# Kernel tuning notes

Measured on AMD Instinct MI355X. Metric: run time of the kernel, lower is better.

## Reference

```python
import jax, jax.numpy as jnp
import numpy as np

P, F_IN, HG, C, T, E, HOUT = 4096, 64, 64, 64, 32, 65536, 12
LEAKY_SLOPE = 0.2
LN_EPS = 1e-5


def setup_inputs() -> dict:
    key = jax.random.key(0)
    ks = jax.random.split(key, 14)
    g = lambda k, shape, scale: (jax.random.normal(k, shape, jnp.float32) * scale)
    return {
        "X": jax.random.normal(ks[0], (1, P, F_IN, T), jnp.float32),
        "edge_index": jax.random.randint(ks[1], (T, 2, E), 0, P, jnp.int32),
        # GATv2 params (single head)
        "Wl": g(ks[2], (F_IN, HG), 0.1),
        "Wr": g(ks[3], (F_IN, HG), 0.1),
        "att": g(ks[4], (HG,), 0.1),
        "gat_b": g(ks[5], (HG,), 0.02),
        # 1x1 time conv (HG -> C) and 1x1 residual conv (F_IN -> C)
        "W_time": g(ks[6], (C, HG), 0.1),
        "b_time": g(ks[7], (C,), 0.02),
        "W_res": g(ks[8], (C, F_IN), 0.1),
        "b_res": g(ks[9], (C,), 0.02),
        # LayerNorm over channel dim C
        "ln_g": jnp.ones((C,), jnp.float32),
        "ln_b": jnp.zeros((C,), jnp.float32),
        # final conv: Conv2d(in=T, out=HOUT, kernel=(1, C)) -> weight (HOUT, T, C)
        "W_final": g(ks[10], (HOUT, T, C), 0.05),
        "b_final": g(ks[11], (HOUT,), 0.02),
    }


def reference(X, edge_index, Wl, Wr, att, gat_b, W_time, b_time, W_res, b_res,
              ln_g, ln_b, W_final, b_final):
    Pn = X.shape[1]

    def gat_t(x, edges):
        # x: (P, F_IN), edges: (2, E) with edges[0]=src j, edges[1]=dst i
        src, dst = edges[0], edges[1]
        hl = x @ Wl                      # (P, HG) messages
        hr = x @ Wr                      # (P, HG) query side
        e = jax.nn.leaky_relu(hl[src] + hr[dst], LEAKY_SLOPE) @ att  # (E,)
        emax = jax.ops.segment_max(e, dst, num_segments=Pn)
        ex = jnp.exp(e - emax[dst])
        den = jax.ops.segment_sum(ex, dst, num_segments=Pn)
        alpha = ex / den[dst]            # softmax over in-edges of each dst
        return jax.ops.segment_sum(alpha[:, None] * hl[src], dst,
                                   num_segments=Pn) + gat_b  # (P, HG)

    xs = jnp.moveaxis(X[0], -1, 0)                     # (T, P, F_IN)
    X_hat = jax.nn.relu(jax.vmap(gat_t)(xs, edge_index))  # (T, P, HG)

    th = jnp.einsum('tph,ch->tpc', X_hat, W_time) + b_time  # time conv 1x1
    rs = jnp.einsum('tpf,cf->tpc', xs, W_res) + b_res       # residual conv 1x1
    y = jax.nn.relu(th + rs)                                 # (T, P, C)

    mu = jnp.mean(y, axis=-1, keepdims=True)
    var = jnp.var(y, axis=-1, keepdims=True)
    yn = (y - mu) * jax.lax.rsqrt(var + LN_EPS) * ln_g + ln_b  # (T, P, C)

    # final conv: in-channels = T, kernel (1, C) -> contract over t and c
    out = jnp.einsum('tpc,otc->po', yn, W_final) + b_final     # (P, HOUT)
    return out[None]                                           # (1, P, HOUT)
```

## Files before the change

### kernel.cpp

```cpp
#include <hip/hip_runtime.h>
#include <math.h>

#define NP 4096
#define F_IN 64
#define HG 64
#define NC 64
#define NT 32
#define NE 65536
#define HOUT 12
#define LEAKY 0.2f
#define LN_EPS 1e-5f
#define CAP 48

template <int CTRL>
__device__ __forceinline__ float dppadd(float v, float x) {
    int r = __builtin_amdgcn_update_dpp(0, __builtin_bit_cast(int, x), CTRL, 0xF, 0xF, false);
    return v + __builtin_bit_cast(float, r);
}
__device__ __forceinline__ float rowsum16(float v) {
    v = dppadd<0x128>(v, v);
    v = dppadd<0x124>(v, v);
    v = dppadd<0x122>(v, v);
    v = dppadd<0x121>(v, v);
    return v;
}
__device__ __forceinline__ float laneXorSum(float v) {
    v += __shfl_xor(v, 16, 64);
    v += __shfl_xor(v, 32, 64);
    return v;
}

#define FMA4(Acomp, B, r)                                                     \
    acc[r][0] += (Acomp) * (B).x; acc[r][1] += (Acomp) * (B).y;               \
    acc[r][2] += (Acomp) * (B).z; acc[r][3] += (Acomp) * (B).w;

__global__ __launch_bounds__(256) void k_front(const float* __restrict__ X,
        const float* __restrict__ Wl, const float* __restrict__ Wr,
        const float* __restrict__ W_res, const float* __restrict__ b_res,
        const float* __restrict__ W_time, const float* __restrict__ bf,
        float* __restrict__ hl, float* __restrict__ hr, float* __restrict__ rs,
        float* __restrict__ wtT, float* __restrict__ out) {
    __shared__ float smem[8960];
    int b = blockIdx.x;
    int tid = threadIdx.x;
    if (b < 2048) {
        float (*xs)[F_IN][36] = (float (*)[F_IN][36])smem;
        float (*bk)[68] = (float (*)[68])(smem + 4608);
        int p0 = b * 2;
        const float4* Xp = (const float4*)(X + (size_t)p0 * F_IN * NT);
        for (int i4 = tid; i4 < 1024; i4 += 256) {
            int pp = i4 >> 9, f = (i4 >> 3) & 63, t0 = (i4 & 7) * 4;
            *(float4*)&xs[pp][f][t0] = Xp[i4];
        }
        int ng = tid & 15, pp = (tid >> 4) & 1, tg = tid >> 5;
        int n0 = ng * 4, t0 = tg * 4;
        {
            const float4* B4 = (const float4*)Wl;
            for (int i4 = tid; i4 < 1024; i4 += 256)
                *(float4*)&bk[i4 >> 4][(i4 & 15) * 4] = B4[i4];
            __syncthreads();
            float acc[4][4];
#pragma unroll
            for (int i = 0; i < 4; ++i)
#pragma unroll
                for (int j2 = 0; j2 < 4; ++j2) acc[i][j2] = 0.f;
#pragma unroll 8
            for (int f = 0; f < F_IN; ++f) {
                float4 B = *(const float4*)&bk[f][n0];
                float4 A = *(const float4*)&xs[pp][f][t0];
                FMA4(A.x, B, 0) FMA4(A.y, B, 1) FMA4(A.z, B, 2) FMA4(A.w, B, 3)
            }
#pragma unroll
            for (int i = 0; i < 4; ++i) {
                float4 v;
                v.x = acc[i][0]; v.y = acc[i][1]; v.z = acc[i][2]; v.w = acc[i][3];
                *(float4*)&hl[((size_t)(t0 + i) * NP + p0 + pp) * HG + n0] = v;
            }
            __syncthreads();
        }
        {
            const float4* B4 = (const float4*)Wr;
            for (int i4 = tid; i4 < 1024; i4 += 256)
                *(float4*)&bk[i4 >> 4][(i4 & 15) * 4] = B4[i4];
            __syncthreads();
            float acc[4][4];
#pragma unroll
            for (int i = 0; i < 4; ++i)
#pragma unroll
                for (int j2 = 0; j2 < 4; ++j2) acc[i][j2] = 0.f;
#pragma unroll 8
            for (int f = 0; f < F_IN; ++f) {
                float4 B = *(const float4*)&bk[f][n0];
                float4 A = *(const float4*)&xs[pp][f][t0];
                FMA4(A.x, B, 0) FMA4(A.y, B, 1) FMA4(A.z, B, 2) FMA4(A.w, B, 3)
            }
#pragma unroll
            for (int i = 0; i < 4; ++i) {
                float4 v;
                v.x = acc[i][0]; v.y = acc[i][1]; v.z = acc[i][2]; v.w = acc[i][3];
                *(float4*)&hr[((size_t)(t0 + i) * NP + p0 + pp) * HG + n0] = v;
            }
            __syncthreads();
        }
        {
            for (int i = tid; i < F_IN * NC; i += 256) {
                int c = i >> 6, f = i & 63;
                bk[f][c] = W_res[i];
            }
            __syncthreads();
            float4 br4 = *(const float4*)&b_res[n0];
            float acc[4][4];
#pragma unroll
            for (int i = 0; i < 4; ++i) {
                acc[i][0] = br4.x; acc[i][1] = br4.y; acc[i][2] = br4.z; acc[i][3] = br4.w;
            }
#pragma unroll 8
            for (int f = 0; f < F_IN; ++f) {
                float4 B = *(const float4*)&bk[f][n0];
                float4 A = *(const float4*)&xs[pp][f][t0];
                FMA4(A.x, B, 0) FMA4(A.y, B, 1) FMA4(A.z, B, 2) FMA4(A.w, B, 3)
            }
#pragma unroll
            for (int i = 0; i < 4; ++i) {
                float4 v;
                v.x = acc[i][0]; v.y = acc[i][1]; v.z = acc[i][2]; v.w = acc[i][3];
                *(float4*)&rs[((size_t)(t0 + i) * NP + p0 + pp) * NC + n0] = v;
            }
        }
    } else if (b < 2064) {
        int i = (b - 2048) * 256 + tid;
        wtT[i] = W_time[(i & 63) * 64 + (i >> 6)];
    } else {
        int i = (b - 2064) * 256 + tid;
        out[i] = bf[i % HOUT];
    }
}

__global__ __launch_bounds__(512) void k_build(const int* __restrict__ EI,
        int* __restrict__ cnt, unsigned short* __restrict__ scap) {
    __shared__ unsigned short buck[512][CAP];
    __shared__ int cnts[512];
    int b = blockIdx.x;
    int t = (b & 7) + 8 * ((b >> 3) & 3);
    int r = b >> 5;
    int tid = threadIdx.x;
    cnts[tid] = 0;
    __syncthreads();
    const int4* srcA = (const int4*)(EI + (size_t)t * 2 * NE);
    const int4* dstA = (const int4*)(EI + (size_t)t * 2 * NE + NE);
    for (int i = tid; i < NE / 4; i += 512) {
        int4 s = srcA[i];
        int4 d = dstA[i];
        if ((d.x >> 9) == r) { int lo = d.x & 511; int sl = atomicAdd(&cnts[lo], 1); if (sl < CAP) buck[lo][sl] = (unsigned short)s.x; }
        if ((d.y >> 9) == r) { int lo = d.y & 511; int sl = atomicAdd(&cnts[lo], 1); if (sl < CAP) buck[lo][sl] = (unsigned short)s.y; }
        if ((d.z >> 9) == r) { int lo = d.z & 511; int sl = atomicAdd(&cnts[lo], 1); if (sl < CAP) buck[lo][sl] = (unsigned short)s.z; }
        if ((d.w >> 9) == r) { int lo = d.w & 511; int sl = atomicAdd(&cnts[lo], 1); if (sl < CAP) buck[lo][sl] = (unsigned short)s.w; }
    }
    __syncthreads();
    cnt[(t << 12) + (r << 9) + tid] = cnts[tid];
    unsigned int* dstw = (unsigned int*)(scap + ((size_t)((t << 12) + (r << 9))) * CAP);
    const unsigned int* srcw = (const unsigned int*)buck;
    for (int i = tid; i < 512 * CAP / 2; i += 512)
        dstw[i] = srcw[i];
}

__global__ __launch_bounds__(256) void k_gat(const float* __restrict__ hl,
        float* __restrict__ hr,
        const int* __restrict__ cnt, const unsigned short* __restrict__ scap,
        const float* __restrict__ att, const float* __restrict__ gat_b) {
    __shared__ int sidx[4][64];
    int b = blockIdx.x;
    int k = b >> 3;
    int t = (b & 7) + 8 * (k >> 10);
    int ws = threadIdx.x >> 6;
    int i = (k & 1023) * 4 + ws;
    int lane = threadIdx.x & 63;
    int row = lane >> 4;
    int c0 = (lane & 15) * 4;
    size_t nbase = ((size_t)t * NP + i) * HG;
    const float* hlt = hl + (size_t)t * NP * HG;
    float4 r4 = *(const float4*)&hr[nbase + c0];
    float4 at4 = *(const float4*)&att[c0];
    int deg = cnt[(t << 12) + i];
    deg = (deg < CAP) ? deg : CAP;
    const unsigned short* sp = scap + ((size_t)((t << 12) + i)) * CAP;
    int stage = (lane < deg) ? lane : 0;
    sidx[ws][lane] = (int)sp[stage];
    float l = 0.f;
    float4 acc = {0.f, 0.f, 0.f, 0.f};
    int nfull = deg & ~7;
    int j = 0;
    for (; j < nfull; j += 8) {
        int src0 = sidx[ws][j + row];
        int src1 = sidx[ws][j + 4 + row];
        float4 h0 = *(const float4*)&hlt[((size_t)src0 << 6) + c0];
        float4 h1 = *(const float4*)&hlt[((size_t)src1 << 6) + c0];
        float4 z0, z1;
        z0.x = h0.x + r4.x; z0.y = h0.y + r4.y; z0.z = h0.z + r4.z; z0.w = h0.w + r4.w;
        z1.x = h1.x + r4.x; z1.y = h1.y + r4.y; z1.z = h1.z + r4.z; z1.w = h1.w + r4.w;
        z0.x = fmaxf(z0.x, LEAKY * z0.x); z0.y = fmaxf(z0.y, LEAKY * z0.y);
        z0.z = fmaxf(z0.z, LEAKY * z0.z); z0.w = fmaxf(z0.w, LEAKY * z0.w);
        z1.x = fmaxf(z1.x, LEAKY * z1.x); z1.y = fmaxf(z1.y, LEAKY * z1.y);
        z1.z = fmaxf(z1.z, LEAKY * z1.z); z1.w = fmaxf(z1.w, LEAKY * z1.w);
        float e0 = rowsum16(z0.x * at4.x + z0.y * at4.y + z0.z * at4.z + z0.w * at4.w);
        float e1 = rowsum16(z1.x * at4.x + z1.y * at4.y + z1.z * at4.z + z1.w * at4.w);
        float w0 = __expf(e0);
        float w1 = __expf(e1);
        l += w0 + w1;
        acc.x += w0 * h0.x + w1 * h1.x;
        acc.y += w0 * h0.y + w1 * h1.y;
        acc.z += w0 * h0.z + w1 * h1.z;
        acc.w += w0 * h0.w + w1 * h1.w;
    }
    for (; j < deg; j += 4) {
        int jj = j + row;
        int src = sidx[ws][(jj < deg) ? jj : 0];
        float4 ha = *(const float4*)&hlt[((size_t)src << 6) + c0];
        float4 za;
        za.x = ha.x + r4.x; za.y = ha.y + r4.y; za.z = ha.z + r4.z; za.w = ha.w + r4.w;
        za.x = fmaxf(za.x, LEAKY * za.x);
        za.y = fmaxf(za.y, LEAKY * za.y);
        za.z = fmaxf(za.z, LEAKY * za.z);
        za.w = fmaxf(za.w, LEAKY * za.w);
        float ep = za.x * at4.x + za.y * at4.y + za.z * at4.z + za.w * at4.w;
        float e = rowsum16(ep);
        float w = __expf(e);
        w = (jj < deg) ? w : 0.f;
        l += w;
        acc.x += w * ha.x; acc.y += w * ha.y; acc.z += w * ha.z; acc.w += w * ha.w;
    }
    float lt = laneXorSum(l);
    acc.x = laneXorSum(acc.x);
    acc.y = laneXorSum(acc.y);
    acc.z = laneXorSum(acc.z);
    acc.w = laneXorSum(acc.w);
    if (row == 0) {
        float inv = (deg > 0) ? (1.0f / lt) : 0.f;
        float4 gb = *(const float4*)&gat_b[c0];
        float4 o;
        o.x = fmaxf(acc.x * inv + gb.x, 0.f);
        o.y = fmaxf(acc.y * inv + gb.y, 0.f);
        o.z = fmaxf(acc.z * inv + gb.z, 0.f);
        o.w = fmaxf(acc.w * inv + gb.w, 0.f);
        *(float4*)&hr[nbase + c0] = o;
    }
}

__global__ __launch_bounds__(256) void k_pf(const float* __restrict__ Xhat,
        const float* __restrict__ wtT, const float* __restrict__ b_time,
        const float* __restrict__ rs, const float* __restrict__ ln_g,
        const float* __restrict__ ln_b, const float* __restrict__ Wf,
        float* __restrict__ out) {
    __shared__ float in_t[64][68];
    __shared__ float bk[64][68];
    int bx = blockIdx.x;
    int tc = bx & 7;
    int p0 = (bx >> 3) * 64;
    int tid = threadIdx.x;
    const float4* wsrc = (const float4*)wtT;
    for (int i4 = tid; i4 < 1024; i4 += 256) {
        int h = i4 >> 4, c4 = (i4 & 15) * 4;
        *(float4*)&bk[h][c4] = wsrc[i4];
    }
    int cg = tid & 15, pg = tid >> 4;
    int c0 = cg * 4, pl = pg * 4;
    float4 bt4 = *(const float4*)&b_time[c0];
    float4 lg = *(const float4*)&ln_g[c0];
    float4 lb = *(const float4*)&ln_b[c0];
    float ot[4][HOUT];
#pragma unroll
    for (int i = 0; i < 4; ++i)
#pragma unroll
        for (int o = 0; o < HOUT; ++o) ot[i][o] = 0.f;
    for (int ti = 0; ti < 4; ++ti) {
        int t = tc + ti * 8;
        __syncthreads();
        const float4* src = (const float4*)(Xhat + ((size_t)t * NP + p0) * HG);
        for (int i4 = tid; i4 < 1024; i4 += 256) {
            int pp = i4 >> 4, c4 = (i4 & 15) * 4;
            *(float4*)&in_t[pp][c4] = src[i4];
        }
        __syncthreads();
        float acc[4][4];
#pragma unroll
        for (int i = 0; i < 4; ++i) {
            acc[i][0] = bt4.x; acc[i][1] = bt4.y; acc[i][2] = bt4.z; acc[i][3] = bt4.w;
        }
#pragma unroll
        for (int k4 = 0; k4 < 16; ++k4) {
            float4 A0 = *(const float4*)&in_t[pl + 0][k4 * 4];
            float4 A1 = *(const float4*)&in_t[pl + 1][k4 * 4];
            float4 A2 = *(const float4*)&in_t[pl + 2][k4 * 4];
            float4 A3 = *(const float4*)&in_t[pl + 3][k4 * 4];
            float4 B0 = *(const float4*)&bk[k4 * 4 + 0][c0];
            FMA4(A0.x, B0, 0) FMA4(A1.x, B0, 1) FMA4(A2.x, B0, 2) FMA4(A3.x, B0, 3)
            float4 B1 = *(const float4*)&bk[k4 * 4 + 1][c0];
            FMA4(A0.y, B1, 0) FMA4(A1.y, B1, 1) FMA4(A2.y, B1, 2) FMA4(A3.y, B1, 3)
            float4 B2 = *(const float4*)&bk[k4 * 4 + 2][c0];
            FMA4(A0.z, B2, 0) FMA4(A1.z, B2, 1) FMA4(A2.z, B2, 2) FMA4(A3.z, B2, 3)
            float4 B3 = *(const float4*)&bk[k4 * 4 + 3][c0];
            FMA4(A0.w, B3, 0) FMA4(A1.w, B3, 1) FMA4(A2.w, B3, 2) FMA4(A3.w, B3, 3)
        }
        float4 ynv[4];
#pragma unroll
        for (int i = 0; i < 4; ++i) {
            size_t prow = (size_t)t * NP + p0 + pl + i;
            float4 r4 = *(const float4*)&rs[prow * NC + c0];
            float y0 = fmaxf(acc[i][0] + r4.x, 0.f), y1 = fmaxf(acc[i][1] + r4.y, 0.f);
            float y2 = fmaxf(acc[i][2] + r4.z, 0.f), y3 = fmaxf(acc[i][3] + r4.w, 0.f);
            float s = rowsum16(y0 + y1 + y2 + y3);
            float ss = rowsum16(y0 * y0 + y1 * y1 + y2 * y2 + y3 * y3);
            float mu = s * (1.f / 64.f);
            float var = ss * (1.f / 64.f) - mu * mu;
            float rsd = rsqrtf(var + LN_EPS);
            ynv[i].x = (y0 - mu) * rsd * lg.x + lb.x;
            ynv[i].y = (y1 - mu) * rsd * lg.y + lb.y;
            ynv[i].z = (y2 - mu) * rsd * lg.z + lb.z;
            ynv[i].w = (y3 - mu) * rsd * lg.w + lb.w;
        }
#pragma unroll
        for (int o = 0; o < HOUT; ++o) {
            float4 w4 = *(const float4*)&Wf[(size_t)o * NT * NC + t * NC + c0];
#pragma unroll
            for (int i = 0; i < 4; ++i)
                ot[i][o] += ynv[i].x * w4.x + ynv[i].y * w4.y
                          + ynv[i].z * w4.z + ynv[i].w * w4.w;
        }
    }
#pragma unroll
    for (int i = 0; i < 4; ++i)
#pragma unroll
        for (int o = 0; o < HOUT; ++o) ot[i][o] = rowsum16(ot[i][o]);
    if (cg == 0) {
#pragma unroll
        for (int i = 0; i < 4; ++i) {
            int p = p0 + pl + i;
#pragma unroll
            for (int o = 0; o < HOUT; ++o)
                atomicAdd(&out[p * HOUT + o], ot[i][o]);
        }
    }
}

extern "C" void kernel_launch(void* const* d_in, const int* in_sizes, int n_in,
                              void* d_out, int out_size, void* d_ws, size_t ws_size,
                              hipStream_t stream) {
    const float* X      = (const float*)d_in[0];
    const int*   EI     = (const int*)d_in[1];
    const float* Wl     = (const float*)d_in[2];
    const float* Wr     = (const float*)d_in[3];
    const float* att    = (const float*)d_in[4];
    const float* gat_b  = (const float*)d_in[5];
    const float* W_time = (const float*)d_in[6];
    const float* b_time = (const float*)d_in[7];
    const float* W_res  = (const float*)d_in[8];
    const float* b_res  = (const float*)d_in[9];
    const float* ln_g   = (const float*)d_in[10];
    const float* ln_b   = (const float*)d_in[11];
    const float* Wf     = (const float*)d_in[12];
    const float* bf     = (const float*)d_in[13];
    float* out = (float*)d_out;

    char* ws = (char*)d_ws;
    const size_t MB = 1024 * 1024;
    float* hl   = (float*)(ws);
    float* hr   = (float*)(ws + 32 * MB);
    float* rs   = (float*)(ws + 64 * MB);
    int*   cnt  = (int*)  (ws + 96 * MB);
    float* wtT  = (float*)(ws + 96 * MB + 512 * 1024);
    unsigned short* scap = (unsigned short*)(ws + 97 * MB);

    k_front<<<2256, 256, 0, stream>>>(X, Wl, Wr, W_res, b_res, W_time, bf,
                                      hl, hr, rs, wtT, out);
    k_build<<<256, 512, 0, stream>>>(EI, cnt, scap);
    k_gat  <<<(NT * NP) / 4, 256, 0, stream>>>(hl, hr, cnt, scap, att, gat_b);
    k_pf   <<<512, 256, 0, stream>>>(hr, wtT, b_time, rs, ln_g, ln_b, Wf, out);
}
```

Baseline: 283.5 us.

## Fuse edge-bucket build into front kernel with split edge halves, widen final pass

Moves the CSR-style in-edge bucket construction into the front kernel as extra 256-thread blocks, so one launch disappears and the edge sorting overlaps with the projection GEMMs. Each block now scans half of the edge list into its own 32-slot bucket, and the GAT kernel merges the two halves per destination, capping total degree at 64. The final projection kernel is also split over 16 time groups instead of 8, doubling its block count. In exchange the GAT kernel does more index arithmetic, and the final kernel issues more atomic adds to the output.

```diff
diff --git a/kernel.cpp b/kernel.cpp
--- a/kernel.cpp
+++ b/kernel.cpp
@@ -10,7 +10,7 @@
 #define HOUT 12
 #define LEAKY 0.2f
 #define LN_EPS 1e-5f
-#define CAP 48
+#define CAPC 32
 
 template <int CTRL>
 __device__ __forceinline__ float dppadd(float v, float x) {
@@ -38,15 +38,43 @@
         const float* __restrict__ Wl, const float* __restrict__ Wr,
         const float* __restrict__ W_res, const float* __restrict__ b_res,
         const float* __restrict__ W_time, const float* __restrict__ bf,
+        const int* __restrict__ EI,
         float* __restrict__ hl, float* __restrict__ hr, float* __restrict__ rs,
-        float* __restrict__ wtT, float* __restrict__ out) {
+        float* __restrict__ wtT, float* __restrict__ out,
+        int* __restrict__ cnt, unsigned short* __restrict__ scap) {
     __shared__ float smem[8960];
     int b = blockIdx.x;
     int tid = threadIdx.x;
-    if (b < 2048) {
+    if (b < 512) {
+        unsigned short (*buck)[CAPC] = (unsigned short (*)[CAPC])smem;
+        int* cnts = (int*)(smem + 8192);
+        int t = (b & 7) + 8 * ((b >> 3) & 3);
+        int rem = b >> 5;
+        int c = rem & 1, r = rem >> 1;
+        cnts[tid] = 0; cnts[tid + 256] = 0;
+        __syncthreads();
+        const int4* srcA = (const int4*)(EI + (size_t)t * 2 * NE) + c * (NE / 8);
+        const int4* dstA = (const int4*)(EI + (size_t)t * 2 * NE + NE) + c * (NE / 8);
+        for (int i = tid; i < NE / 8; i += 256) {
+            int4 s = srcA[i];
+            int4 d = dstA[i];
+            if ((d.x >> 9) == r) { int lo = d.x & 511; int sl = atomicAdd(&cnts[lo], 1); if (sl < CAPC) buck[lo][sl] = (unsigned short)s.x; }
+            if ((d.y >> 9) == r) { int lo = d.y & 511; int sl = atomicAdd(&cnts[lo], 1); if (sl < CAPC) buck[lo][sl] = (unsigned short)s.y; }
+            if ((d.z >> 9) == r) { int lo = d.z & 511; int sl = atomicAdd(&cnts[lo], 1); if (sl < CAPC) buck[lo][sl] = (unsigned short)s.z; }
+            if ((d.w >> 9) == r) { int lo = d.w & 511; int sl = atomicAdd(&cnts[lo], 1); if (sl < CAPC) buck[lo][sl] = (unsigned short)s.w; }
+        }
+        __syncthreads();
+        int obase = ((t * 2 + c) << 12) + (r << 9);
+        cnt[obase + tid] = cnts[tid];
+        cnt[obase + tid + 256] = cnts[tid + 256];
+        unsigned int* dstw = (unsigned int*)(scap + (size_t)obase * CAPC);
+        const unsigned int* srcw = (const unsigned int*)buck;
+        for (int i = tid; i < 512 * CAPC / 2; i += 256)
+            dstw[i] = srcw[i];
+    } else if (b < 2560) {
         float (*xs)[F_IN][36] = (float (*)[F_IN][36])smem;
         float (*bk)[68] = (float (*)[68])(smem + 4608);
-        int p0 = b * 2;
+        int p0 = (b - 512) * 2;
         const float4* Xp = (const float4*)(X + (size_t)p0 * F_IN * NT);
         for (int i4 = tid; i4 < 1024; i4 += 256) {
             int pp = i4 >> 9, f = (i4 >> 3) & 63, t0 = (i4 & 7) * 4;
@@ -127,41 +155,13 @@
                 *(float4*)&rs[((size_t)(t0 + i) * NP + p0 + pp) * NC + n0] = v;
             }
         }
-    } else if (b < 2064) {
-        int i = (b - 2048) * 256 + tid;
+    } else if (b < 2576) {
+        int i = (b - 2560) * 256 + tid;
         wtT[i] = W_time[(i & 63) * 64 + (i >> 6)];
     } else {
-        int i = (b - 2064) * 256 + tid;
+        int i = (b - 2576) * 256 + tid;
         out[i] = bf[i % HOUT];
     }
-}
-
-__global__ __launch_bounds__(512) void k_build(const int* __restrict__ EI,
-        int* __restrict__ cnt, unsigned short* __restrict__ scap) {
-    __shared__ unsigned short buck[512][CAP];
-    __shared__ int cnts[512];
-    int b = blockIdx.x;
-    int t = (b & 7) + 8 * ((b >> 3) & 3);
-    int r = b >> 5;
-    int tid = threadIdx.x;
-    cnts[tid] = 0;
-    __syncthreads();
-    const int4* srcA = (const int4*)(EI + (size_t)t * 2 * NE);
-    const int4* dstA = (const int4*)(EI + (size_t)t * 2 * NE + NE);
-    for (int i = tid; i < NE / 4; i += 512) {
-        int4 s = srcA[i];
-        int4 d = dstA[i];
-        if ((d.x >> 9) == r) { int lo = d.x & 511; int sl = atomicAdd(&cnts[lo], 1); if (sl < CAP) buck[lo][sl] = (unsigned short)s.x; }
-        if ((d.y >> 9) == r) { int lo = d.y & 511; int sl = atomicAdd(&cnts[lo], 1); if (sl < CAP) buck[lo][sl] = (unsigned short)s.y; }
-        if ((d.z >> 9) == r) { int lo = d.z & 511; int sl = atomicAdd(&cnts[lo], 1); if (sl < CAP) buck[lo][sl] = (unsigned short)s.z; }
-        if ((d.w >> 9) == r) { int lo = d.w & 511; int sl = atomicAdd(&cnts[lo], 1); if (sl < CAP) buck[lo][sl] = (unsigned short)s.w; }
-    }
-    __syncthreads();
-    cnt[(t << 12) + (r << 9) + tid] = cnts[tid];
-    unsigned int* dstw = (unsigned int*)(scap + ((size_t)((t << 12) + (r << 9))) * CAP);
-    const unsigned int* srcw = (const unsigned int*)buck;
-    for (int i = tid; i < 512 * CAP / 2; i += 512)
-        dstw[i] = srcw[i];
 }
 
 __global__ __launch_bounds__(256) void k_gat(const float* __restrict__ hl,
@@ -181,11 +181,16 @@
     const float* hlt = hl + (size_t)t * NP * HG;
     float4 r4 = *(const float4*)&hr[nbase + c0];
     float4 at4 = *(const float4*)&att[c0];
-    int deg = cnt[(t << 12) + i];
-    deg = (deg < CAP) ? deg : CAP;
-    const unsigned short* sp = scap + ((size_t)((t << 12) + i)) * CAP;
-    int stage = (lane < deg) ? lane : 0;
-    sidx[ws][lane] = (int)sp[stage];
+    int d0 = cnt[((t * 2 + 0) << 12) + i]; d0 = (d0 < CAPC) ? d0 : CAPC;
+    int d1 = cnt[((t * 2 + 1) << 12) + i]; d1 = (d1 < CAPC) ? d1 : CAPC;
+    int deg = d0 + d1;
+    deg = (deg < 64) ? deg : 64;
+    const unsigned short* s0 = scap + ((size_t)(((t * 2 + 0) << 12) + i)) * CAPC;
+    const unsigned short* s1 = scap + ((size_t)(((t * 2 + 1) << 12) + i)) * CAPC;
+    int li = (lane < deg) ? lane : 0;
+    int f1 = (li >= d0);
+    int idx = f1 ? (li - d0) : li;
+    sidx[ws][lane] = (int)(f1 ? s1 : s0)[idx];
     float l = 0.f;
     float4 acc = {0.f, 0.f, 0.f, 0.f};
     int nfull = deg & ~7;
@@ -254,8 +259,8 @@
     __shared__ float in_t[64][68];
     __shared__ float bk[64][68];
     int bx = blockIdx.x;
-    int tc = bx & 7;
-    int p0 = (bx >> 3) * 64;
+    int tc = bx & 15;
+    int p0 = (bx >> 4) * 64;
     int tid = threadIdx.x;
     const float4* wsrc = (const float4*)wtT;
     for (int i4 = tid; i4 < 1024; i4 += 256) {
@@ -272,8 +277,8 @@
     for (int i = 0; i < 4; ++i)
 #pragma unroll
         for (int o = 0; o < HOUT; ++o) ot[i][o] = 0.f;
-    for (int ti = 0; ti < 4; ++ti) {
-        int t = tc + ti * 8;
+    for (int ti = 0; ti < 2; ++ti) {
+        int t = tc + ti * 16;
         __syncthreads();
         const float4* src = (const float4*)(Xhat + ((size_t)t * NP + p0) * HG);
         for (int i4 = tid; i4 < 1024; i4 += 256) {
@@ -366,13 +371,12 @@
     float* hl   = (float*)(ws);
     float* hr   = (float*)(ws + 32 * MB);
     float* rs   = (float*)(ws + 64 * MB);
-    int*   cnt  = (int*)  (ws + 96 * MB);
-    float* wtT  = (float*)(ws + 96 * MB + 512 * 1024);
-    unsigned short* scap = (unsigned short*)(ws + 97 * MB);
-
-    k_front<<<2256, 256, 0, stream>>>(X, Wl, Wr, W_res, b_res, W_time, bf,
-                                      hl, hr, rs, wtT, out);
-    k_build<<<256, 512, 0, stream>>>(EI, cnt, scap);
+    float* wtT  = (float*)(ws + 96 * MB);
+    int*   cnt  = (int*)  (ws + 97 * MB);
+    unsigned short* scap = (unsigned short*)(ws + 98 * MB);
+
+    k_front<<<2768, 256, 0, stream>>>(X, Wl, Wr, W_res, b_res, W_time, bf, EI,
+                                      hl, hr, rs, wtT, out, cnt, scap);
     k_gat  <<<(NT * NP) / 4, 256, 0, stream>>>(hl, hr, cnt, scap, att, gat_b);
-    k_pf   <<<512, 256, 0, stream>>>(hr, wtT, b_time, rs, ln_g, ln_b, Wf, out);
-}
+    k_pf   <<<1024, 256, 0, stream>>>(hr, wtT, b_time, rs, ln_g, ln_b, Wf, out);
+}
```

After: 285.3 us. About the same (+0.6%).
